# Kernel tuning notes

Measured on AMD Instinct MI355X. Metric: run time of the kernel, lower is better.

Reference implementation:

```python
import jax, jax.numpy as jnp
import numpy as np
import math

# static config
NH, HD, HID = 16, 128, 2048
ROT = 64            # head_dim * partial_rotary_factor(0.5)
EPS = 1e-6
GROUPS = 8
CHUNK = 64
THETA = 10000.0
LAYER_IDX, N_LAYERS = 1, 32
B, S = 2, 2048


def _base_slopes(n):
    # power-of-two branch of HF ALiBi slopes
    start = 2 ** (-(2 ** (-(math.log2(n) - 3))))
    return [start * (start ** i) for i in range(n)]

# per-head log-decay (negative): slope = -base * (1 - (l-1)/(L-1) + 1e-5)
SLOPE = jnp.asarray(
    -np.array(_base_slopes(NH), dtype=np.float32)
    * (1.0 - (LAYER_IDX - 1) / (N_LAYERS - 1) + 1e-5),
    dtype=jnp.float32)  # [NH]


def _rmsnorm(x, w):
    return x * jax.lax.rsqrt(jnp.mean(x * x, axis=-1, keepdims=True) + EPS) * w


def _partial_rope(x, positions):
    # x: [B,S,NH,HD]; neox-style rotary on first ROT dims, rest passthrough
    half = ROT // 2
    inv_freq = 1.0 / (THETA ** (jnp.arange(half, dtype=jnp.float32) / half))
    ang = positions.astype(jnp.float32)[:, None] * inv_freq       # [S, half]
    cos = jnp.cos(ang)[None, :, None, :]
    sin = jnp.sin(ang)[None, :, None, :]
    x1, x2, rest = x[..., :half], x[..., half:ROT], x[..., ROT:]
    return jnp.concatenate(
        [x1 * cos - x2 * sin, x2 * cos + x1 * sin, rest], axis=-1)


def setup_inputs() -> dict:
    key = jax.random.key(0)
    ks = jax.random.split(key, 4)
    return {
        'positions': jnp.arange(S, dtype=jnp.int32),
        'hidden_states': jax.random.normal(ks[0], (B, S, HID), jnp.float32),
        'recurrent_state': jnp.zeros((B, NH, HD, HD), jnp.float32),
        'w_qkv': jax.random.normal(ks[1], (HID, 3 * NH * HD), jnp.float32) * 0.02,
        'w_g': jax.random.normal(ks[2], (HID, NH * HD), jnp.float32) * 0.02,
        'w_dense': jax.random.normal(ks[3], (NH * HD, HID), jnp.float32) * 0.02,
        'q_norm_w': jnp.ones((HD,), jnp.float32),
        'k_norm_w': jnp.ones((HD,), jnp.float32),
        'g_norm_w': jnp.ones((NH * HD,), jnp.float32),
    }


def reference(positions, hidden_states, recurrent_state, w_qkv, w_g, w_dense,
              q_norm_w, k_norm_w, g_norm_w):
    # fused QKV projection
    qkv = hidden_states @ w_qkv                       # [B,S,3*NH*HD]
    q, k, v = jnp.split(qkv, 3, axis=-1)
    q = q.reshape(B, S, NH, HD)
    k = k.reshape(B, S, NH, HD)
    v = v.reshape(B, S, NH, HD)

    # QK RMSNorm then partial rotary
    q = _partial_rope(_rmsnorm(q, q_norm_w), positions)
    k = _partial_rope(_rmsnorm(k, k_norm_w), positions)

    # chunked ALiBi-decayed linear attention:
    #   S_t = lam * S_{t-1} + k_t v_t^T ; o_t = q_t S_t, lam = exp(slope)
    NC = S // CHUNK
    qc = q.reshape(B, NC, CHUNK, NH, HD).transpose(1, 0, 3, 2, 4)  # [NC,B,NH,C,HD]
    kc = k.reshape(B, NC, CHUNK, NH, HD).transpose(1, 0, 3, 2, 4)
    vc = v.reshape(B, NC, CHUNK, NH, HD).transpose(1, 0, 3, 2, 4)

    t = jnp.arange(CHUNK, dtype=jnp.float32)
    # intra-chunk causal decay mask lam^(i-j), i>=j: [NH,C,C]
    dec_mask = jnp.where(t[:, None] >= t[None, :],
                         jnp.exp(SLOPE[:, None, None] * (t[:, None] - t[None, :])),
                         0.0)
    q_dec = jnp.exp(SLOPE[:, None] * (t[None, :] + 1.0))            # [NH,C] lam^(i+1)
    k_dec = jnp.exp(SLOPE[:, None] * (CHUNK - 1.0 - t[None, :]))    # [NH,C] lam^(C-1-j)
    lam_C = jnp.exp(SLOPE * CHUNK)                                   # [NH]

    def step(state, inp):
        qb, kb, vb = inp                                  # [B,NH,C,HD]
        scores = jnp.einsum('bhid,bhjd->bhij', qb, kb) * dec_mask[None]
        o_intra = jnp.einsum('bhij,bhjd->bhid', scores, vb)
        o_inter = jnp.einsum('bhid,bhde->bhie', qb * q_dec[None, :, :, None], state)
        new_state = (state * lam_C[None, :, None, None]
                     + jnp.einsum('bhjd,bhje->bhde', kb * k_dec[None, :, :, None], vb))
        return new_state, o_intra + o_inter

    _, o = jax.lax.scan(step, recurrent_state, (qc, kc, vc))  # o: [NC,B,NH,C,HD]
    o = o.transpose(1, 0, 3, 2, 4).reshape(B, S, NH * HD)

    # GroupRMSNorm on attention output, sigmoid gate, output projection
    og = o.reshape(B, S, GROUPS, (NH * HD) // GROUPS)
    og = og * jax.lax.rsqrt(jnp.mean(og * og, axis=-1, keepdims=True) + EPS)
    o = og.reshape(B, S, NH * HD) * g_norm_w
    o = o * jax.nn.sigmoid(hidden_states @ w_g)
    return o @ w_dense
```

## Files before the change

kernel.cpp:

```cpp
#include <hip/hip_runtime.h>
#include <hip/hip_bf16.h>
#include <math.h>

#define NH   16
#define HD   128
#define HID  2048
#define NKV  6144
#define B_   2
#define S_   2048
#define NC   32
#define CHUNK_ 64
#define GROUPS_ 8

typedef __bf16 bf16_t;
typedef bf16_t bf16x8 __attribute__((ext_vector_type(8)));
typedef float  f32x4  __attribute__((ext_vector_type(4)));

__device__ __forceinline__ float b2f(unsigned int u) {
    union { unsigned int u; float f; } c; c.u = (u & 0xffffu) << 16; return c.f;
}
__device__ __forceinline__ unsigned int f2b(float f) {
    union { float f; unsigned int u; } c; c.f = f;
    unsigned int u = c.u;
    return (u + 0x7fffu + ((u >> 16) & 1u)) >> 16;
}

#define GLOAD_LDS16(gp, lp) __builtin_amdgcn_global_load_lds(                     \
    (const __attribute__((address_space(1))) void*)(gp),                          \
    (__attribute__((address_space(3))) void*)(lp), 16, 0, 0)

__global__ __launch_bounds__(256) void cvt_bf16(const float* __restrict__ in,
                                                unsigned short* __restrict__ out, int n8)
{
    int i = blockIdx.x * 256 + threadIdx.x;
    if (i >= n8) return;
    const float4* p = (const float4*)in + (size_t)i * 2;
    float4 a = p[0], b = p[1];
    uint4 o;
    o.x = f2b(a.x) | (f2b(a.y) << 16);
    o.y = f2b(a.z) | (f2b(a.w) << 16);
    o.z = f2b(b.x) | (f2b(b.y) << 16);
    o.w = f2b(b.z) | (f2b(b.w) << 16);
    ((uint4*)out)[i] = o;
}

__global__ __launch_bounds__(256) void transpose_cvt(const float* __restrict__ in,
                                                     unsigned short* __restrict__ out,
                                                     int Kdim, int Ndim)
{
    __shared__ float tile[32][33];
    int ntx = Ndim >> 5;
    int bx = blockIdx.x % ntx;
    int by = blockIdx.x / ntx;
    int lx = threadIdx.x & 31, ly = threadIdx.x >> 5;
    int r0 = by * 32, c0 = bx * 32;
    #pragma unroll
    for (int r = 0; r < 4; ++r)
        tile[ly + r * 8][lx] = in[(size_t)(r0 + ly + r * 8) * Ndim + c0 + lx];
    __syncthreads();
    #pragma unroll
    for (int r = 0; r < 4; ++r)
        out[(size_t)(c0 + ly + r * 8) * Kdim + r0 + lx] = (unsigned short)f2b(tile[lx][ly + r * 8]);
}

__device__ __forceinline__ void storeOne(float* p, float v) { *p = v; }
__device__ __forceinline__ void storeOne(unsigned short* p, float v) { *p = (unsigned short)f2b(v); }

template <typename OutT>
__global__ __launch_bounds__(256) void gemm_mfma(const bf16_t* __restrict__ A,
                                                 const bf16_t* __restrict__ Bt,
                                                 OutT* __restrict__ C,
                                                 int M, int N, int K)
{
    __shared__ bf16_t As[128 * 32];
    __shared__ bf16_t Bs[128 * 32];
    int tid  = threadIdx.x;
    int ntiles = N >> 7;
    int bx = blockIdx.x % ntiles;
    int by = blockIdx.x / ntiles;
    int lane = tid & 63;
    int wave = tid >> 6;
    int wm = (wave >> 1) * 64;
    int wn = (wave & 1) * 64;
    int l16  = lane & 15;
    int quad = lane >> 4;

    f32x4 acc[4][4];
    #pragma unroll
    for (int i = 0; i < 4; ++i)
        #pragma unroll
        for (int j = 0; j < 4; ++j) { f32x4 z = {0.f, 0.f, 0.f, 0.f}; acc[i][j] = z; }

    const bf16_t* aG = A  + (size_t)(by * 128 + (tid >> 2)) * K + (tid & 3) * 8;
    const bf16_t* bG = Bt + (size_t)(bx * 128 + (tid >> 2)) * K + (tid & 3) * 8;
    bf16_t* aL0 = As + tid * 8;
    bf16_t* aL1 = As + 2048 + tid * 8;
    bf16_t* bL0 = Bs + tid * 8;
    bf16_t* bL1 = Bs + 2048 + tid * 8;
    const size_t half = (size_t)64 * K;

    for (int kt = 0; kt < K; kt += 32) {
        GLOAD_LDS16(aG + kt,        aL0);
        GLOAD_LDS16(aG + half + kt, aL1);
        GLOAD_LDS16(bG + kt,        bL0);
        GLOAD_LDS16(bG + half + kt, bL1);
        __syncthreads();
        bf16x8 af[4], bf[4];
        #pragma unroll
        for (int t = 0; t < 4; ++t) {
            af[t] = *(const bf16x8*)(As + (wm + t * 16 + l16) * 32 + quad * 8);
            bf[t] = *(const bf16x8*)(Bs + (wn + t * 16 + l16) * 32 + quad * 8);
        }
        #pragma unroll
        for (int mt = 0; mt < 4; ++mt)
            #pragma unroll
            for (int nt = 0; nt < 4; ++nt)
                acc[mt][nt] = __builtin_amdgcn_mfma_f32_16x16x32_bf16(af[mt], bf[nt], acc[mt][nt], 0, 0, 0);
        __syncthreads();
    }

    #pragma unroll
    for (int mt = 0; mt < 4; ++mt)
        #pragma unroll
        for (int nt = 0; nt < 4; ++nt) {
            int col = bx * 128 + wn + nt * 16 + l16;
            #pragma unroll
            for (int r = 0; r < 4; ++r) {
                int row = by * 128 + wm + mt * 16 + quad * 4 + r;
                storeOne(C + (size_t)row * N + col, acc[mt][nt][r]);
            }
        }
}


__device__ __forceinline__ void ld_fr4(bf16x8 (&d)[4][2], const bf16_t* b, int s0, int ri) {
    #pragma unroll
    for (int i = 0; i < 4; ++i)
        #pragma unroll
        for (int k = 0; k < 2; ++k)
            d[i][k] = *(const bf16x8*)(b + (((s0 + i) * 2 + k) << 9) + ri);
}
__device__ __forceinline__ void ld_fr2(bf16x8 (&d)[2][2], const bf16_t* b, int s0, int ri) {
    #pragma unroll
    for (int i = 0; i < 2; ++i)
        #pragma unroll
        for (int k = 0; k < 2; ++k)
            d[i][k] = *(const bf16x8*)(b + (((s0 + i) * 2 + k) << 9) + ri);
}
__device__ __forceinline__ void mfma_quad(f32x4 (&a)[4][2], const bf16x8 (&af)[4][2],
                                          const bf16x8 (&bv)[2][2]) {
    #pragma unroll
    for (int mt = 0; mt < 4; ++mt)
        #pragma unroll
        for (int nt = 0; nt < 2; ++nt)
            #pragma unroll
            for (int ks = 0; ks < 2; ++ks)
                a[mt][nt] = __builtin_amdgcn_mfma_f32_16x16x32_bf16(af[mt][ks], bv[nt][ks], a[mt][nt], 0, 0, 0);
}

#define BAR()     asm volatile("s_barrier" ::: "memory")
#define PRIO1()   __builtin_amdgcn_s_setprio(1)
#define PRIO0()   __builtin_amdgcn_s_setprio(0)
#define SCHEDB()  __builtin_amdgcn_sched_barrier(0)
#define VMCNT6()  asm volatile("s_waitcnt vmcnt(6)" ::: "memory")
#define VMCNT0()  asm volatile("s_waitcnt vmcnt(0)" ::: "memory")

__global__ __launch_bounds__(512, 2) void gemm_qg_256(const bf16_t* __restrict__ A,
                                                      const bf16_t* __restrict__ Bt,
                                                      unsigned short* __restrict__ Cq,
                                                      unsigned short* __restrict__ Cg)
{
    __shared__ bf16_t Asm[2][2][8192];
    __shared__ bf16_t Bsm[2][2][8192];
    const int K  = HID;
    const int NT = K / 64;

    int tid  = threadIdx.x;
    int wave = tid >> 6, lane = tid & 63;
    int wm = wave >> 2, wn = wave & 3;
    int l16 = lane & 15, quad = lane >> 4;
    int wm4 = wm * 4, wn2 = wn * 2;

    int bid = blockIdx.x;
    int xcd = bid & 7, idx = bid >> 3;
    int by  = (xcd >> 2) * 8 + (idx >> 3);
    int bx  = (xcd & 3) * 8 + (idx & 7);

    int rd_in = ((l16 << 5) | (quad << 3)) ^ (((l16 >> 3) & 1) << 4);

    int ch = lane ^ ((lane & 32) >> 4);
    int rr = ch >> 2;
    int cc = (ch & 3) * 8;

    const bf16_t* aSrc0 = A  + (size_t)(by * 256 +       wave * 16 + rr) * K + cc;
    const bf16_t* aSrc1 = A  + (size_t)(by * 256 + 128 + wave * 16 + rr) * K + cc;
    const bf16_t* bSrc0 = Bt + (size_t)(bx * 256 +       wave * 16 + rr) * K + cc;
    const bf16_t* bSrc1 = Bt + (size_t)(bx * 256 + 128 + wave * 16 + rr) * K + cc;

#define STAGE_A(h, t) do {                                                        \
        const bf16_t* _g = ((h) ? aSrc1 : aSrc0) + (size_t)(t) * 64;              \
        bf16_t* _l = &Asm[(t) & 1][(h)][wave * 1024 + lane * 8];                  \
        GLOAD_LDS16(_g,      _l);                                                 \
        GLOAD_LDS16(_g + 32, _l + 512); } while (0)
#define STAGE_B(h, t) do {                                                        \
        const bf16_t* _g = ((h) ? bSrc1 : bSrc0) + (size_t)(t) * 64;              \
        bf16_t* _l = &Bsm[(t) & 1][(h)][wave * 1024 + lane * 8];                  \
        GLOAD_LDS16(_g,      _l);                                                 \
        GLOAD_LDS16(_g + 32, _l + 512); } while (0)

    f32x4 acc[2][2][4][2];
    #pragma unroll
    for (int a0 = 0; a0 < 2; ++a0)
        #pragma unroll
        for (int a1 = 0; a1 < 2; ++a1)
            #pragma unroll
            for (int a2 = 0; a2 < 4; ++a2)
                #pragma unroll
                for (int a3 = 0; a3 < 2; ++a3) { f32x4 z = {0.f,0.f,0.f,0.f}; acc[a0][a1][a2][a3] = z; }

    bf16x8 afA[4][2], afB[4][2];
    bf16x8 bf0[2][2], bf1[2][2];

    STAGE_A(0, 0); STAGE_B(0, 0); STAGE_B(1, 0); STAGE_A(1, 0);
    STAGE_A(0, 1); STAGE_B(1, 1); STAGE_A(1, 1);
    VMCNT6();
    BAR();
    ld_fr4(afA, &Asm[0][0][0], wm4, rd_in);
    ld_fr2(bf1, &Bsm[0][1][0], wn2, rd_in);
    ld_fr2(bf0, &Bsm[0][0][0], wn2, rd_in);

    #pragma unroll 2
    for (int t = 0; t < NT - 2; ++t) {
        const int buf = t & 1, nbuf = buf ^ 1;
        STAGE_B(0, t + 1);
        BAR();
        PRIO1(); mfma_quad(acc[0][0], afA, bf0); PRIO0();
        BAR();
        ld_fr4(afB, &Asm[buf][1][0], wm4, rd_in);
        STAGE_A(0, t + 2);
        SCHEDB();
        BAR();
        PRIO1(); mfma_quad(acc[0][1], afA, bf1); PRIO0();
        BAR();
        STAGE_B(1, t + 2);
        BAR();
        PRIO1(); mfma_quad(acc[1][1], afB, bf1); PRIO0();
        BAR();
        STAGE_A(1, t + 2);
        VMCNT6();
        BAR();
        ld_fr4(afA, &Asm[nbuf][0][0], wm4, rd_in);
        ld_fr2(bf1, &Bsm[nbuf][1][0], wn2, rd_in);
        SCHEDB();
        PRIO1(); mfma_quad(acc[1][0], afB, bf0); PRIO0();
        ld_fr2(bf0, &Bsm[nbuf][0][0], wn2, rd_in);
        BAR();
    }
    {
        const int t = NT - 2, buf = t & 1, nbuf = buf ^ 1;
        STAGE_B(0, t + 1);
        BAR();
        PRIO1(); mfma_quad(acc[0][0], afA, bf0); PRIO0();
        BAR();
        ld_fr4(afB, &Asm[buf][1][0], wm4, rd_in);
        SCHEDB();
        BAR();
        PRIO1(); mfma_quad(acc[0][1], afA, bf1); PRIO0();
        BAR();
        PRIO1(); mfma_quad(acc[1][1], afB, bf1); PRIO0();
        VMCNT0();
        BAR();
        ld_fr4(afA, &Asm[nbuf][0][0], wm4, rd_in);
        ld_fr2(bf1, &Bsm[nbuf][1][0], wn2, rd_in);
        SCHEDB();
        PRIO1(); mfma_quad(acc[1][0], afB, bf0); PRIO0();
        ld_fr2(bf0, &Bsm[nbuf][0][0], wn2, rd_in);
        BAR();
    }
    {
        const int buf = (NT - 1) & 1;
        PRIO1(); mfma_quad(acc[0][0], afA, bf0); PRIO0();
        ld_fr4(afB, &Asm[buf][1][0], wm4, rd_in);
        SCHEDB();
        PRIO1(); mfma_quad(acc[0][1], afA, bf1); PRIO0();
        PRIO1(); mfma_quad(acc[1][1], afB, bf1); PRIO0();
        PRIO1(); mfma_quad(acc[1][0], afB, bf0); PRIO0();
    }
#undef STAGE_A
#undef STAGE_B

    unsigned short* Cc; int Nn, colbase;
    if (bx < 24) { Cc = Cq; Nn = NKV; colbase = bx * 256; }
    else         { Cc = Cg; Nn = HID; colbase = bx * 256 - NKV; }
    int row0 = by * 256 + wm * 64 + quad * 4;
    int col0 = colbase + wn * 32 + l16;
    #pragma unroll
    for (int mh = 0; mh < 2; ++mh)
        #pragma unroll
        for (int nh = 0; nh < 2; ++nh)
            #pragma unroll
            for (int mt = 0; mt < 4; ++mt)
                #pragma unroll
                for (int nt = 0; nt < 2; ++nt) {
                    int col = col0 + nh * 128 + nt * 16;
                    #pragma unroll
                    for (int r = 0; r < 4; ++r) {
                        int row = row0 + mh * 128 + mt * 16 + r;
                        Cc[(size_t)row * Nn + col] = (unsigned short)f2b(acc[mh][nh][mt][nt][r]);
                    }
                }
}

__global__ __launch_bounds__(256) void norm_rope(unsigned short* __restrict__ qkv,
                                                 const int* __restrict__ positions,
                                                 const float* __restrict__ qw,
                                                 const float* __restrict__ kw)
{
    int bs = blockIdx.x;
    int s  = bs & (S_ - 1);
    int tid = threadIdx.x;
    int l16 = tid & 15;
    unsigned short* base = qkv + (size_t)bs * NKV;
    float pos = (float)positions[s];

    #pragma unroll
    for (int p = 0; p < 2; ++p) {
        int rr = p * 16 + (tid >> 4);
        int qk = rr >> 4;
        int h  = rr & 15;
        unsigned short* row = base + qk * HID + h * HD;
        const float* w = qk ? kw : qw;
        uint4 v = *(const uint4*)(row + l16 * 8);
        float x[8];
        x[0] = b2f(v.x); x[1] = b2f(v.x >> 16);
        x[2] = b2f(v.y); x[3] = b2f(v.y >> 16);
        x[4] = b2f(v.z); x[5] = b2f(v.z >> 16);
        x[6] = b2f(v.w); x[7] = b2f(v.w >> 16);
        float ss = 0.f;
        #pragma unroll
        for (int t = 0; t < 8; ++t) ss += x[t] * x[t];
        ss += __shfl_xor(ss, 1); ss += __shfl_xor(ss, 2);
        ss += __shfl_xor(ss, 4); ss += __shfl_xor(ss, 8);
        float inv = rsqrtf(ss * (1.0f / 128.0f) + 1e-6f);
        float n[8];
        #pragma unroll
        for (int t = 0; t < 8; ++t) n[t] = x[t] * inv * w[l16 * 8 + t];
        float pr[8];
        #pragma unroll
        for (int t = 0; t < 8; ++t) pr[t] = __shfl_xor(n[t], 4);
        if (l16 < 8) {
            #pragma unroll
            for (int t = 0; t < 8; ++t) {
                int dim = l16 * 8 + t;
                int i = dim & 31;
                float ang = pos * exp2f(-(float)i * 0.4152410118609203f);
                float cs = cosf(ang), sn = sinf(ang);
                n[t] = (dim < 32) ? (n[t] * cs - pr[t] * sn) : (n[t] * cs + pr[t] * sn);
            }
        }
        uint4 o;
        o.x = f2b(n[0]) | (f2b(n[1]) << 16);
        o.y = f2b(n[2]) | (f2b(n[3]) << 16);
        o.z = f2b(n[4]) | (f2b(n[5]) << 16);
        o.w = f2b(n[6]) | (f2b(n[7]) << 16);
        *(uint4*)(row + l16 * 8) = o;
    }
}

__global__ __launch_bounds__(256) void chunk_kv(const unsigned short* __restrict__ qkv,
                                                unsigned short* __restrict__ wbuf)
{
    __shared__ unsigned short kt[128 * 72];
    __shared__ unsigned short vt[128 * 72];
    int bi = blockIdx.x;
    int c = bi & 31, bh = bi >> 5, h = bh & 15, b = bh >> 4;
    int tid = threadIdx.x;
    float slope = -exp2f(-0.5f * (float)(h + 1)) * (1.0f + 1e-5f);

    const unsigned short* kbase = qkv + ((size_t)(b * S_ + c * CHUNK_)) * NKV + HID + h * HD;
    const unsigned short* vbase = kbase + HID;

    for (int idx = tid; idx < 4096; idx += 256) {
        int j = idx >> 6, p = idx & 63;
        unsigned int ku = *(const unsigned int*)(kbase + (size_t)j * NKV + p * 2);
        kt[(2 * p) * 72 + j]     = (unsigned short)(ku & 0xffffu);
        kt[(2 * p + 1) * 72 + j] = (unsigned short)(ku >> 16);
        float kd = expf(slope * (float)(63 - j));
        unsigned int vu = *(const unsigned int*)(vbase + (size_t)j * NKV + p * 2);
        vt[(2 * p) * 72 + j]     = (unsigned short)f2b(b2f(vu) * kd);
        vt[(2 * p + 1) * 72 + j] = (unsigned short)f2b(b2f(vu >> 16) * kd);
    }
    __syncthreads();

    int lane = tid & 63, wave = tid >> 6;
    int wm = (wave >> 1) * 64;
    int wn = (wave & 1) * 64;
    int l16 = lane & 15, quad = lane >> 4;

    f32x4 acc[4][4];
    #pragma unroll
    for (int i = 0; i < 4; ++i)
        #pragma unroll
        for (int j = 0; j < 4; ++j) { f32x4 z = {0.f,0.f,0.f,0.f}; acc[i][j] = z; }

    #pragma unroll
    for (int ks = 0; ks < 64; ks += 32) {
        bf16x8 af[4], bf[4];
        #pragma unroll
        for (int t = 0; t < 4; ++t) {
            af[t] = *(const bf16x8*)((const bf16_t*)vt + (wm + t * 16 + l16) * 72 + ks + quad * 8);
            bf[t] = *(const bf16x8*)((const bf16_t*)kt + (wn + t * 16 + l16) * 72 + ks + quad * 8);
        }
        #pragma unroll
        for (int mt = 0; mt < 4; ++mt)
            #pragma unroll
            for (int nt = 0; nt < 4; ++nt)
                acc[mt][nt] = __builtin_amdgcn_mfma_f32_16x16x32_bf16(af[mt], bf[nt], acc[mt][nt], 0, 0, 0);
    }

    unsigned short* wp = wbuf + ((size_t)bi << 14);
    #pragma unroll
    for (int mt = 0; mt < 4; ++mt)
        #pragma unroll
        for (int nt = 0; nt < 4; ++nt) {
            int dcol = wn + nt * 16 + l16;
            #pragma unroll
            for (int r = 0; r < 4; ++r) {
                int erow = wm + mt * 16 + quad * 4 + r;
                wp[(size_t)erow * 128 + dcol] = (unsigned short)f2b(acc[mt][nt][r]);
            }
        }
}

__global__ __launch_bounds__(256) void state_scan(const unsigned short* __restrict__ wbuf,
                                                  const float* __restrict__ rs0,
                                                  unsigned short* __restrict__ stbuf)
{
    int bi = blockIdx.x;
    int es = bi & 15, bh = bi >> 4, h = bh & 15, b = bh >> 4;
    int tid = threadIdx.x;
    float slope = -exp2f(-0.5f * (float)(h + 1)) * (1.0f + 1e-5f);
    float lam = expf(slope * 64.0f);

    int e  = es * 8 + (tid >> 5);
    int d0 = (tid & 31) * 4;

    float S[4];
    const float* rp = rs0 + ((size_t)(b * NH + h)) * HD * HD + e;
    #pragma unroll
    for (int t = 0; t < 4; ++t) S[t] = rp[(size_t)(d0 + t) * HD];

    size_t off = (size_t)e * 128 + d0;
    for (int c = 0; c < NC; ++c) {
        size_t base = (((size_t)bh * NC + c) << 14) + off;
        uint2 o;
        o.x = f2b(S[0]) | (f2b(S[1]) << 16);
        o.y = f2b(S[2]) | (f2b(S[3]) << 16);
        *(uint2*)(stbuf + base) = o;
        uint2 w = *(const uint2*)(wbuf + base);
        S[0] = S[0] * lam + b2f(w.x);
        S[1] = S[1] * lam + b2f(w.x >> 16);
        S[2] = S[2] * lam + b2f(w.y);
        S[3] = S[3] * lam + b2f(w.y >> 16);
    }
}

__global__ __launch_bounds__(256) void chunk_out(const unsigned short* __restrict__ qkv,
                                                 const unsigned short* __restrict__ stbuf,
                                                 unsigned short* __restrict__ obuf)
{
    __shared__ unsigned short qs[64 * 136];
    __shared__ unsigned short vt[128 * 72];
    __shared__ unsigned short sc[64 * 72];

    int bi = blockIdx.x;
    int c = bi & 31, bh = bi >> 5, h = bh & 15, b = bh >> 4;
    int tid = threadIdx.x;
    float slope = -exp2f(-0.5f * (float)(h + 1)) * (1.0f + 1e-5f);

    int lane = tid & 63, wave = tid >> 6;
    int l16 = lane & 15, quad = lane >> 4;
    int wn3 = wave * 32;

    const unsigned short* stp = stbuf + (((size_t)bh * NC + c) << 14);
    bf16x8 bsf[4][2];
    #pragma unroll
    for (int ksp4 = 0; ksp4 < 4; ++ksp4)
        #pragma unroll
        for (int nt = 0; nt < 2; ++nt)
            bsf[ksp4][nt] = *(const bf16x8*)((const bf16_t*)stp +
                (size_t)(wn3 + nt * 16 + l16) * 128 + ksp4 * 32 + quad * 8);

    const unsigned short* qrow = qkv + ((size_t)(b * S_ + c * CHUNK_)) * NKV + h * HD;
    const unsigned short* krow = qrow + HID;
    for (int idx = tid; idx < 1024; idx += 256) {
        int row = idx >> 4, c8 = (idx & 15) * 8;
        *(uint4*)(qs + row * 136 + c8) = *(const uint4*)(qrow + (size_t)row * NKV + c8);
    }
    const unsigned short* vbase = qrow + 2 * HID;
    for (int idx = tid; idx < 4096; idx += 256) {
        int j = idx >> 6, p = idx & 63;
        unsigned int vu = *(const unsigned int*)(vbase + (size_t)j * NKV + p * 2);
        vt[(2 * p) * 72 + j]     = (unsigned short)(vu & 0xffffu);
        vt[(2 * p + 1) * 72 + j] = (unsigned short)(vu >> 16);
    }
    __syncthreads();

    {
        f32x4 accS[4];
        #pragma unroll
        for (int t = 0; t < 4; ++t) { f32x4 z = {0.f,0.f,0.f,0.f}; accS[t] = z; }
        #pragma unroll
        for (int ksp = 0; ksp < 128; ksp += 32) {
            bf16x8 aq = *(const bf16x8*)((const bf16_t*)qs + (wave * 16 + l16) * 136 + ksp + quad * 8);
            #pragma unroll
            for (int nt = 0; nt < 4; ++nt) {
                bf16x8 bk = *(const bf16x8*)((const bf16_t*)krow + (size_t)(nt * 16 + l16) * NKV + ksp + quad * 8);
                accS[nt] = __builtin_amdgcn_mfma_f32_16x16x32_bf16(aq, bk, accS[nt], 0, 0, 0);
            }
        }
        float ad[4];
        #pragma unroll
        for (int r = 0; r < 4; ++r) ad[r] = expf(slope * (float)(wave * 16 + quad * 4 + r));
        #pragma unroll
        for (int nt = 0; nt < 4; ++nt) {
            int j = nt * 16 + l16;
            float bd = expf(-slope * (float)j);
            #pragma unroll
            for (int r = 0; r < 4; ++r) {
                int i = wave * 16 + quad * 4 + r;
                float v = (i >= j) ? accS[nt][r] * ad[r] * bd : 0.0f;
                sc[i * 72 + j] = (unsigned short)f2b(v);
            }
        }
    }
    __syncthreads();

    f32x4 accI[4][2], accE[4][2];
    #pragma unroll
    for (int i = 0; i < 4; ++i)
        #pragma unroll
        for (int j = 0; j < 2; ++j) { f32x4 z = {0.f,0.f,0.f,0.f}; accI[i][j] = z; accE[i][j] = z; }

    #pragma unroll
    for (int ksp = 0; ksp < 64; ksp += 32) {
        bf16x8 as[4], bv[2];
        #pragma unroll
        for (int mt = 0; mt < 4; ++mt)
            as[mt] = *(const bf16x8*)((const bf16_t*)sc + (mt * 16 + l16) * 72 + ksp + quad * 8);
        #pragma unroll
        for (int nt = 0; nt < 2; ++nt)
            bv[nt] = *(const bf16x8*)((const bf16_t*)vt + (wn3 + nt * 16 + l16) * 72 + ksp + quad * 8);
        #pragma unroll
        for (int mt = 0; mt < 4; ++mt)
            #pragma unroll
            for (int nt = 0; nt < 2; ++nt)
                accI[mt][nt] = __builtin_amdgcn_mfma_f32_16x16x32_bf16(as[mt], bv[nt], accI[mt][nt], 0, 0, 0);
    }
    #pragma unroll
    for (int ksp4 = 0; ksp4 < 4; ++ksp4) {
        bf16x8 aq[4];
        #pragma unroll
        for (int mt = 0; mt < 4; ++mt)
            aq[mt] = *(const bf16x8*)((const bf16_t*)qs + (mt * 16 + l16) * 136 + ksp4 * 32 + quad * 8);
        #pragma unroll
        for (int mt = 0; mt < 4; ++mt)
            #pragma unroll
            for (int nt = 0; nt < 2; ++nt)
                accE[mt][nt] = __builtin_amdgcn_mfma_f32_16x16x32_bf16(aq[mt], bsf[ksp4][nt], accE[mt][nt], 0, 0, 0);
    }

    #pragma unroll
    for (int mt = 0; mt < 4; ++mt) {
        #pragma unroll
        for (int r = 0; r < 4; ++r) {
            int i = mt * 16 + quad * 4 + r;
            float qd = expf(slope * (float)(i + 1));
            int orow = b * S_ + c * CHUNK_ + i;
            #pragma unroll
            for (int nt = 0; nt < 2; ++nt) {
                int col = h * HD + wn3 + nt * 16 + l16;
                float o = accI[mt][nt][r] + qd * accE[mt][nt][r];
                obuf[(size_t)orow * 2048 + col] = (unsigned short)f2b(o);
            }
        }
    }
}

__global__ __launch_bounds__(256) void gnorm_gate(const unsigned short* __restrict__ o,
                                                  unsigned short* __restrict__ gate,
                                                  const float* __restrict__ gw)
{
    int row = blockIdx.x >> 3;
    int g   = blockIdx.x & 7;
    int col = g * 256 + threadIdx.x;
    size_t idx = (size_t)row * 2048 + col;
    float ov = b2f(o[idx]);
    float ss = ov * ov;
    #pragma unroll
    for (int off = 32; off > 0; off >>= 1) ss += __shfl_xor(ss, off);
    __shared__ float part[4];
    if ((threadIdx.x & 63) == 0) part[threadIdx.x >> 6] = ss;
    __syncthreads();
    float tot = part[0] + part[1] + part[2] + part[3];
    float inv = rsqrtf(tot * (1.0f / 256.0f) + 1e-6f);
    float gv = b2f(gate[idx]);
    float sig = 1.0f / (1.0f + expf(-gv));
    gate[idx] = (unsigned short)f2b(ov * inv * gw[col] * sig);
}

extern "C" void kernel_launch(void* const* d_in, const int* in_sizes, int n_in,
                              void* d_out, int out_size, void* d_ws, size_t ws_size,
                              hipStream_t stream) {
    const int*   positions = (const int*)d_in[0];
    const float* hidden    = (const float*)d_in[1];
    const float* rstate    = (const float*)d_in[2];
    const float* w_qkv     = (const float*)d_in[3];
    const float* w_g       = (const float*)d_in[4];
    const float* w_dense   = (const float*)d_in[5];
    const float* q_norm_w  = (const float*)d_in[6];
    const float* k_norm_w  = (const float*)d_in[7];
    const float* g_norm_w  = (const float*)d_in[8];
    float* out = (float*)d_out;

    const int MR = B_ * S_;

    char* w = (char*)d_ws;
    unsigned short* qkv  = (unsigned short*)w;            w += (size_t)MR * NKV * 2;
    unsigned short* gbuf = (unsigned short*)w;            w += (size_t)MR * 2048 * 2;
    unsigned short* wdT  = (unsigned short*)w;            w += (size_t)HID * HID * 2;
    char* regionA = w;                                    w += (size_t)MR * HID * 2 + (size_t)8192 * HID * 2;
    char* regionB = w;
    unsigned short* hbf   = (unsigned short*)regionA;
    unsigned short* btQG  = (unsigned short*)(regionA + (size_t)MR * HID * 2);
    unsigned short* wqT   = btQG;
    unsigned short* wgT   = btQG + (size_t)NKV * HID;
    unsigned short* stbuf = (unsigned short*)regionA;
    unsigned short* wbuf  = (unsigned short*)regionB;
    unsigned short* obuf  = (unsigned short*)regionB;

    cvt_bf16<<<dim3((MR * HID / 8 + 255) / 256), dim3(256), 0, stream>>>(hidden, hbf, MR * HID / 8);
    transpose_cvt<<<dim3((HID / 32) * (NKV / 32)), dim3(256), 0, stream>>>(w_qkv, wqT, HID, NKV);
    transpose_cvt<<<dim3((HID / 32) * (HID / 32)), dim3(256), 0, stream>>>(w_g, wgT, HID, HID);
    transpose_cvt<<<dim3((HID / 32) * (HID / 32)), dim3(256), 0, stream>>>(w_dense, wdT, HID, HID);

    gemm_qg_256<<<dim3(512), dim3(512), 0, stream>>>(
        (const bf16_t*)hbf, (const bf16_t*)btQG, qkv, gbuf);
    norm_rope<<<dim3(B_ * S_), dim3(256), 0, stream>>>(qkv, positions, q_norm_w, k_norm_w);

    chunk_kv<<<dim3(B_ * NH * NC), dim3(256), 0, stream>>>(qkv, wbuf);
    state_scan<<<dim3(B_ * NH * 16), dim3(256), 0, stream>>>(wbuf, rstate, stbuf);
    chunk_out<<<dim3(B_ * NH * NC), dim3(256), 0, stream>>>(qkv, stbuf, obuf);

    gnorm_gate<<<dim3(MR * GROUPS_), dim3(256), 0, stream>>>(obuf, gbuf, g_norm_w);
    gemm_mfma<float><<<dim3((MR / 128) * (HID / 128)), dim3(256), 0, stream>>>(
        (const bf16_t*)gbuf, (const bf16_t*)wdT, out, MR, HID, HID);
}
```

Baseline: 464.7 us.

## Simplify QG GEMM main loop to plain double-buffered prefetch

```diff
diff --git a/kernel.cpp b/kernel.cpp
--- a/kernel.cpp
+++ b/kernel.cpp
@@ -159,10 +159,6 @@
 }
 
 #define BAR()     asm volatile("s_barrier" ::: "memory")
-#define PRIO1()   __builtin_amdgcn_s_setprio(1)
-#define PRIO0()   __builtin_amdgcn_s_setprio(0)
-#define SCHEDB()  __builtin_amdgcn_sched_barrier(0)
-#define VMCNT6()  asm volatile("s_waitcnt vmcnt(6)" ::: "memory")
 #define VMCNT0()  asm volatile("s_waitcnt vmcnt(0)" ::: "memory")
 
 __global__ __launch_bounds__(512, 2) void gemm_qg_256(const bf16_t* __restrict__ A,
@@ -218,73 +214,39 @@
                 #pragma unroll
                 for (int a3 = 0; a3 < 2; ++a3) { f32x4 z = {0.f,0.f,0.f,0.f}; acc[a0][a1][a2][a3] = z; }
 
-    bf16x8 afA[4][2], afB[4][2];
-    bf16x8 bf0[2][2], bf1[2][2];
-
-    STAGE_A(0, 0); STAGE_B(0, 0); STAGE_B(1, 0); STAGE_A(1, 0);
-    STAGE_A(0, 1); STAGE_B(1, 1); STAGE_A(1, 1);
-    VMCNT6();
+    STAGE_A(0, 0); STAGE_B(0, 0); STAGE_A(1, 0); STAGE_B(1, 0);
+    VMCNT0();
     BAR();
-    ld_fr4(afA, &Asm[0][0][0], wm4, rd_in);
-    ld_fr2(bf1, &Bsm[0][1][0], wn2, rd_in);
-    ld_fr2(bf0, &Bsm[0][0][0], wn2, rd_in);
 
     #pragma unroll 2
-    for (int t = 0; t < NT - 2; ++t) {
-        const int buf = t & 1, nbuf = buf ^ 1;
-        STAGE_B(0, t + 1);
-        BAR();
-        PRIO1(); mfma_quad(acc[0][0], afA, bf0); PRIO0();
-        BAR();
-        ld_fr4(afB, &Asm[buf][1][0], wm4, rd_in);
-        STAGE_A(0, t + 2);
-        SCHEDB();
-        BAR();
-        PRIO1(); mfma_quad(acc[0][1], afA, bf1); PRIO0();
-        BAR();
-        STAGE_B(1, t + 2);
-        BAR();
-        PRIO1(); mfma_quad(acc[1][1], afB, bf1); PRIO0();
-        BAR();
-        STAGE_A(1, t + 2);
-        VMCNT6();
-        BAR();
-        ld_fr4(afA, &Asm[nbuf][0][0], wm4, rd_in);
-        ld_fr2(bf1, &Bsm[nbuf][1][0], wn2, rd_in);
-        SCHEDB();
-        PRIO1(); mfma_quad(acc[1][0], afB, bf0); PRIO0();
-        ld_fr2(bf0, &Bsm[nbuf][0][0], wn2, rd_in);
-        BAR();
-    }
-    {
-        const int t = NT - 2, buf = t & 1, nbuf = buf ^ 1;
-        STAGE_B(0, t + 1);
-        BAR();
-        PRIO1(); mfma_quad(acc[0][0], afA, bf0); PRIO0();
-        BAR();
-        ld_fr4(afB, &Asm[buf][1][0], wm4, rd_in);
-        SCHEDB();
-        BAR();
-        PRIO1(); mfma_quad(acc[0][1], afA, bf1); PRIO0();
-        BAR();
-        PRIO1(); mfma_quad(acc[1][1], afB, bf1); PRIO0();
+    for (int t = 0; t < NT - 1; ++t) {
+        const int buf = t & 1;
+        STAGE_A(0, t + 1); STAGE_B(0, t + 1); STAGE_A(1, t + 1); STAGE_B(1, t + 1);
+        {
+            bf16x8 afA[4][2], afB[4][2], bf0[2][2], bf1[2][2];
+            ld_fr4(afA, &Asm[buf][0][0], wm4, rd_in);
+            ld_fr2(bf0, &Bsm[buf][0][0], wn2, rd_in);
+            mfma_quad(acc[0][0], afA, bf0);
+            ld_fr2(bf1, &Bsm[buf][1][0], wn2, rd_in);
+            mfma_quad(acc[0][1], afA, bf1);
+            ld_fr4(afB, &Asm[buf][1][0], wm4, rd_in);
+            mfma_quad(acc[1][1], afB, bf1);
+            mfma_quad(acc[1][0], afB, bf0);
+        }
         VMCNT0();
         BAR();
-        ld_fr4(afA, &Asm[nbuf][0][0], wm4, rd_in);
-        ld_fr2(bf1, &Bsm[nbuf][1][0], wn2, rd_in);
-        SCHEDB();
-        PRIO1(); mfma_quad(acc[1][0], afB, bf0); PRIO0();
-        ld_fr2(bf0, &Bsm[nbuf][0][0], wn2, rd_in);
-        BAR();
     }
     {
         const int buf = (NT - 1) & 1;
-        PRIO1(); mfma_quad(acc[0][0], afA, bf0); PRIO0();
+        bf16x8 afA[4][2], afB[4][2], bf0[2][2], bf1[2][2];
+        ld_fr4(afA, &Asm[buf][0][0], wm4, rd_in);
+        ld_fr2(bf0, &Bsm[buf][0][0], wn2, rd_in);
+        mfma_quad(acc[0][0], afA, bf0);
+        ld_fr2(bf1, &Bsm[buf][1][0], wn2, rd_in);
+        mfma_quad(acc[0][1], afA, bf1);
         ld_fr4(afB, &Asm[buf][1][0], wm4, rd_in);
-        SCHEDB();
-        PRIO1(); mfma_quad(acc[0][1], afA, bf1); PRIO0();
-        PRIO1(); mfma_quad(acc[1][1], afB, bf1); PRIO0();
-        PRIO1(); mfma_quad(acc[1][0], afB, bf0); PRIO0();
+        mfma_quad(acc[1][1], afB, bf1);
+        mfma_quad(acc[1][0], afB, bf0);
     }
 #undef STAGE_A
 #undef STAGE_B
```

Result: no change. 459.0 us (-1.2%).
